# Optimization experiments

Measured on AMD Instinct MI355X. Metric: run time of the kernel, lower is better.

The kernel has to match this reference:

```python
import jax, jax.numpy as jnp
import numpy as np

L, B, T, D, H, F, V = 4, 2, 1024, 1024, 16, 4096, 32000
DH = D // H
POWER = 4
EPS = 1e-6


def _anorm(x, gain):
    # y = g * x / (mean(|x|) + eps)  (L1 'diamond' norm)
    return gain * (x / (jnp.mean(jnp.abs(x), axis=-1, keepdims=True) + EPS))


def _rational_softmax(x):
    s = x / (jnp.abs(x) + 1.0)          # squash to (-1, 1)
    p = ((s + 1.0) * 0.5) ** POWER      # shift to (0,1), sharpen
    return p / (jnp.sum(p, axis=-1, keepdims=True) + EPS)


def setup_inputs() -> dict:
    key = jax.random.key(0)
    ks = jax.random.split(key, 12)
    w = 0.02  # weight scale for stability
    return {
        "idx": jax.random.randint(ks[0], (B, T), 0, V),
        "tok_emb": jax.random.normal(ks[1], (V, D), jnp.float32) * w,
        "pos_emb": jax.random.normal(ks[2], (T, D), jnp.float32) * w,
        "Wq": jax.random.normal(ks[3], (L, D, D), jnp.float32) * w,
        "bq": jnp.zeros((L, D), jnp.float32),
        "Wk": jax.random.normal(ks[4], (L, D, D), jnp.float32) * w,
        "bk": jnp.zeros((L, D), jnp.float32),
        "Wv": jax.random.normal(ks[5], (L, D, D), jnp.float32) * w,
        "bv": jnp.zeros((L, D), jnp.float32),
        "Wo": jax.random.normal(ks[6], (L, D, D), jnp.float32) * w,
        "bo": jnp.zeros((L, D), jnp.float32),
        "score_gain": jnp.full((L,), 4.0, jnp.float32),
        "norm1_gain": jnp.ones((L, D), jnp.float32),
        "norm2_gain": jnp.ones((L, D), jnp.float32),
        "W1": jax.random.normal(ks[7], (L, D, F), jnp.float32) * w,
        "b1": jnp.zeros((L, F), jnp.float32),
        "W2": jax.random.normal(ks[8], (L, F, D), jnp.float32) * w,
        "b2": jnp.zeros((L, D), jnp.float32),
        "final_gain": jnp.ones((D,), jnp.float32),
        "Wlm": jax.random.normal(ks[9], (D, V), jnp.float32) * w,
        "blm": jnp.zeros((V,), jnp.float32),
    }


def _forward(idx, tok_emb, pos_emb, Wq, bq, Wk, bk, Wv, bv, Wo, bo,
             score_gain, norm1_gain, norm2_gain, W1, b1, W2, b2,
             final_gain, Wlm, blm):
    Bx, Tx = idx.shape
    x = tok_emb[idx] + pos_emb[:Tx]                 # [B,T,D]
    mask = jnp.triu(jnp.ones((Tx, Tx), bool), 1)    # causal mask (True = masked)
    for l in range(L):
        # --- algebraic attention ---
        h = _anorm(x, norm1_gain[l])
        q = (h @ Wq[l] + bq[l]).reshape(Bx, Tx, H, DH).transpose(0, 2, 1, 3)
        k = (h @ Wk[l] + bk[l]).reshape(Bx, Tx, H, DH).transpose(0, 2, 1, 3)
        v = (h @ Wv[l] + bv[l]).reshape(Bx, Tx, H, DH).transpose(0, 2, 1, 3)
        scores = jnp.einsum('bhqd,bhkd->bhqk', q, k)
        scores = scores - jnp.mean(scores, axis=-1, keepdims=True)
        mad = jnp.mean(jnp.abs(scores), axis=-1, keepdims=True) + EPS
        scores = (scores / mad) * score_gain[l]
        scores = jnp.where(mask, -1000.0, scores)
        attn = _rational_softmax(scores)
        o = jnp.einsum('bhqk,bhkd->bhqd', attn, v)
        o = o.transpose(0, 2, 1, 3).reshape(Bx, Tx, D)
        x = x + (o @ Wo[l] + bo[l])
        # --- FFN with algebraic ReLU ---
        h = _anorm(x, norm2_gain[l])
        h = jnp.maximum(h @ W1[l] + b1[l], 0.0)
        x = x + (h @ W2[l] + b2[l])
    x = _anorm(x, final_gain)
    return x @ Wlm + blm                            # [B,T,V] logits


def reference(idx, tok_emb, pos_emb, Wq, bq, Wk, bk, Wv, bv, Wo, bo,
              score_gain, norm1_gain, norm2_gain, W1, b1, W2, b2,
              final_gain, Wlm, blm):
    return _forward(idx, tok_emb, pos_emb, Wq, bq, Wk, bk, Wv, bv, Wo, bo,
                    score_gain, norm1_gain, norm2_gain, W1, b1, W2, b2,
                    final_gain, Wlm, blm)
```

## Files before the change

### kernel.cpp

```cpp
#include <hip/hip_runtime.h>

typedef unsigned short u16;
typedef __bf16 bf16x8 __attribute__((ext_vector_type(8)));
typedef float f32x4 __attribute__((ext_vector_type(4)));
typedef unsigned int u32;

#define EPSF 1e-6f

__device__ __forceinline__ u16 f2bf(float f) {
  union { float f; unsigned u; } un; un.f = f;
  unsigned r = un.u + 0x7FFFu + ((un.u >> 16) & 1u);
  return (u16)(r >> 16);
}

__device__ __forceinline__ float block_sum(float v) {
  #pragma unroll
  for (int off = 32; off > 0; off >>= 1) v += __shfl_xor(v, off, 64);
  __shared__ float ws[4];
  const int w = threadIdx.x >> 6;
  __syncthreads();
  if ((threadIdx.x & 63) == 0) ws[w] = v;
  __syncthreads();
  return ws[0] + ws[1] + ws[2] + ws[3];
}

__device__ __forceinline__ void lds_cp16(const void* g, void* l) {
  __builtin_amdgcn_global_load_lds(
      (__attribute__((address_space(1))) void*)g,
      (__attribute__((address_space(3))) void*)l, 16, 0, 0);
}

__global__ __launch_bounds__(256) void embed_norm(
    const int* __restrict__ idx, const float* __restrict__ tok,
    const float* __restrict__ pos, const float* __restrict__ gain,
    float* __restrict__ x, u16* __restrict__ h) {
  const int row = blockIdx.x;
  const int tpos = row & 1023;
  const int token = idx[row];
  const int d = threadIdx.x * 4;
  const float4 a = *(const float4*)(tok + (long)token * 1024 + d);
  const float4 b = *(const float4*)(pos + (long)tpos * 1024 + d);
  float4 o; o.x = a.x + b.x; o.y = a.y + b.y; o.z = a.z + b.z; o.w = a.w + b.w;
  *(float4*)(x + (long)row * 1024 + d) = o;
  float s = fabsf(o.x) + fabsf(o.y) + fabsf(o.z) + fabsf(o.w);
  s = block_sum(s);
  const float scale = 1.0f / (s * (1.0f / 1024.0f) + EPSF);
  const float4 g = *(const float4*)(gain + d);
  ushort4 ov;
  ov.x = f2bf(o.x * g.x * scale);
  ov.y = f2bf(o.y * g.y * scale);
  ov.z = f2bf(o.z * g.z * scale);
  ov.w = f2bf(o.w * g.w * scale);
  *(ushort4*)(h + (long)row * 1024 + d) = ov;
}

__global__ __launch_bounds__(512, 4) void attn_v5(
    const u16* __restrict__ qkv, const u16* __restrict__ v_t,
    u16* __restrict__ obuf, const float* __restrict__ score_gain, int l) {
  __shared__ float red1[2][4][16], red2[2][4][16], red3[2][4][16];
  __shared__ float Ured[2][4][16][68];
  __shared__ u16 Pl[8][640];
  const int qt = blockIdx.x, h = blockIdx.y, b = blockIdx.z;
  const int tid = threadIdx.x, w = tid >> 6, l64 = tid & 63;
  const int lq = l64 & 15, kgrp = l64 >> 4;
  const int wq = w >> 2, tq = w & 3;
  const int qglob = qt * 32 + wq * 16 + lq;
  const int qmax  = qt * 32 + wq * 16 + 15;
  const u16* Qg = qkv + (size_t)b * (1024 * 3072) + h * 64;
  const u16* Kg = Qg + 1024;
  const u16* Vt = v_t + (size_t)(b * 16 + h) * (64 * 1024);
  char* Pw = (char*)&Pl[w][0];

  bf16x8 qB0, qB1;
  {
    const u16* qp = Qg + (size_t)qglob * 3072 + (kgrp << 3);
    qB0 = *(const bf16x8*)qp;
    qB1 = *(const bf16x8*)(qp + 32);
  }

  f32x4 s[16];
  {
    const u16* Ktq = Kg + (size_t)(tq * 32 + lq) * 3072 + (kgrp << 3);
    #pragma unroll
    for (int tl = 0; tl < 16; tl++) {
      const int cst = ((tl >> 1) << 7) + ((tl & 1) << 4);
      const u16* kp = Ktq + (size_t)cst * 3072;
      const bf16x8 k0 = *(const bf16x8*)kp;
      const bf16x8 k1 = *(const bf16x8*)(kp + 32);
      f32x4 d = {0.f, 0.f, 0.f, 0.f};
      d = __builtin_amdgcn_mfma_f32_16x16x32_bf16(k0, qB0, d, 0, 0, 0);
      d = __builtin_amdgcn_mfma_f32_16x16x32_bf16(k1, qB1, d, 0, 0, 0);
      s[tl] = d;
    }
  }

  float ssum = 0.f;
  #pragma unroll
  for (int tl = 0; tl < 16; tl++)
    ssum += (s[tl][0] + s[tl][1]) + (s[tl][2] + s[tl][3]);
  ssum += __shfl_xor(ssum, 16, 64);
  ssum += __shfl_xor(ssum, 32, 64);
  if (l64 < 16) red1[wq][tq][l64] = ssum;
  __syncthreads();
  const float mean = (red1[wq][0][lq] + red1[wq][1][lq] +
                      red1[wq][2][lq] + red1[wq][3][lq]) * (1.0f / 1024.0f);

  float asum = 0.f;
  #pragma unroll
  for (int tl = 0; tl < 16; tl++)
    asum += fabsf(s[tl][0] - mean) + fabsf(s[tl][1] - mean) +
            fabsf(s[tl][2] - mean) + fabsf(s[tl][3] - mean);
  asum += __shfl_xor(asum, 16, 64);
  asum += __shfl_xor(asum, 32, 64);
  if (l64 < 16) red2[wq][tq][l64] = asum;
  __syncthreads();
  const float mad = (red2[wq][0][lq] + red2[wq][1][lq] +
                     red2[wq][2][lq] + red2[wq][3][lq]) * (1.0f / 1024.0f) + EPSF;
  const float gs = score_gain[l] / mad;

  float psum = 0.f;
  #pragma unroll
  for (int tl = 0; tl < 16; tl++) {
    const int tbase = tq * 32 + ((tl >> 1) << 7) + ((tl & 1) << 4);
    #pragma unroll
    for (int j = 0; j < 4; j++) {
      const int t = tbase + (kgrp << 2) + j;
      float sv = (s[tl][j] - mean) * gs;
      if (t > qglob) sv = -1000.0f;
      const float rr = sv / (fabsf(sv) + 1.0f);
      const float a1 = (rr + 1.0f) * 0.5f;
      const float a2 = a1 * a1;
      s[tl][j] = a2 * a2;
      psum += s[tl][j];
    }
  }

  f32x4 U[4] = {};
  {
    const u16* Vtq = Vt + (size_t)lq * 1024 + tq * 32 + (kgrp << 3);
    #pragma unroll
    for (int cc = 0; cc < 8; cc++) {
      const int t0 = tq * 32 + (cc << 7);
      if (t0 <= qmax) {
        bf16x8 vA[4];
        #pragma unroll
        for (int dt = 0; dt < 4; dt++)
          vA[dt] = *(const bf16x8*)(Vtq + (size_t)(dt << 4) * 1024 + (cc << 7));
        #pragma unroll
        for (int half = 0; half < 2; half++) {
          #pragma unroll
          for (int pr = 0; pr < 2; pr++) {
            const u32 pk = (u32)f2bf(s[2 * cc + half][pr * 2]) |
                           ((u32)f2bf(s[2 * cc + half][pr * 2 + 1]) << 16);
            *(u32*)(Pw + lq * 80 + half * 32 + (kgrp << 3) + (pr << 2)) = pk;
          }
        }
        asm volatile("s_waitcnt lgkmcnt(0)" ::: "memory");
        __builtin_amdgcn_sched_barrier(0);
        const bf16x8 pB = *(const bf16x8*)(Pw + lq * 80 + (kgrp << 4));
        #pragma unroll
        for (int dt = 0; dt < 4; dt++)
          U[dt] = __builtin_amdgcn_mfma_f32_16x16x32_bf16(vA[dt], pB, U[dt], 0, 0, 0);
      }
    }
  }

  psum += __shfl_xor(psum, 16, 64);
  psum += __shfl_xor(psum, 32, 64);
  if (l64 < 16) red3[wq][tq][l64] = psum;
  #pragma unroll
  for (int dt = 0; dt < 4; dt++)
    *(float4*)&Ured[wq][tq][lq][(dt << 4) + (kgrp << 2)] = *(const float4*)&U[dt];
  __syncthreads();

  {
    const int qq = tid >> 4, dhseg = (tid & 15) << 2;
    const int fwq = qq >> 4, flq = qq & 15;
    const float fps = red3[fwq][0][flq] + red3[fwq][1][flq] +
                      red3[fwq][2][flq] + red3[fwq][3][flq];
    const float oinv = 1.0f / (fps + EPSF);
    float4 u0 = *(const float4*)&Ured[fwq][0][flq][dhseg];
    const float4 u1 = *(const float4*)&Ured[fwq][1][flq][dhseg];
    const float4 u2 = *(const float4*)&Ured[fwq][2][flq][dhseg];
    const float4 u3 = *(const float4*)&Ured[fwq][3][flq][dhseg];
    u0.x = (u0.x + u1.x + u2.x + u3.x) * oinv;
    u0.y = (u0.y + u1.y + u2.y + u3.y) * oinv;
    u0.z = (u0.z + u1.z + u2.z + u3.z) * oinv;
    u0.w = (u0.w + u1.w + u2.w + u3.w) * oinv;
    ushort4 o;
    o.x = f2bf(u0.x); o.y = f2bf(u0.y); o.z = f2bf(u0.z); o.w = f2bf(u0.w);
    u16* dst = obuf + ((size_t)((b << 10) + qt * 32 + qq) << 10) + (h << 6) + dhseg;
    *(ushort4*)dst = o;
  }
}

__global__ void wconv_all(
    const float* __restrict__ Wq, const float* __restrict__ Wk,
    const float* __restrict__ Wv, const float* __restrict__ Wo,
    const float* __restrict__ W1, const float* __restrict__ W2,
    const float* __restrict__ Wlm,
    u16* __restrict__ wqkv_t, u16* __restrict__ wo_t,
    u16* __restrict__ w1_t, u16* __restrict__ w2_t, u16* __restrict__ wlm_t) {
  __shared__ float tile[64][65];
  const int bid = blockIdx.x;
  const float* src; u16* dst; int R, C, c0, r0;
  if (bid < 4096) {
    const int l = bid >> 10, m = (bid >> 8) & 3, t = bid & 255;
    if (m == 0)      src = Wq + (size_t)l * 1048576;
    else if (m == 1) src = Wk + (size_t)l * 1048576;
    else if (m == 2) src = Wv + (size_t)l * 1048576;
    else             src = Wo + (size_t)l * 1048576;
    dst = (m < 3) ? wqkv_t + ((size_t)l * 3072 + m * 1024) * 1024
                  : wo_t + (size_t)l * 1048576;
    R = 1024; C = 1024; c0 = (t & 15) << 6; r0 = (t >> 4) << 6;
  } else if (bid < 8192) {
    const int i = bid - 4096, l = i >> 10, t = i & 1023;
    src = W1 + (size_t)l * 4194304; dst = w1_t + (size_t)l * 4194304;
    R = 1024; C = 4096; c0 = (t & 63) << 6; r0 = (t >> 6) << 6;
  } else if (bid < 12288) {
    const int i = bid - 8192, l = i >> 10, t = i & 1023;
    src = W2 + (size_t)l * 4194304; dst = w2_t + (size_t)l * 4194304;
    R = 4096; C = 1024; c0 = (t & 15) << 6; r0 = (t >> 4) << 6;
  } else {
    const int i = bid - 12288;
    src = Wlm; dst = wlm_t;
    R = 1024; C = 32000; c0 = (i % 500) << 6; r0 = (i / 500) << 6;
  }
  const int tx = threadIdx.x, ty = threadIdx.y;
  const int cg = (tx & 15) << 2;
  const int rg = tx >> 4;
  #pragma unroll
  for (int i = 0; i < 4; i++) {
    const int row = i * 16 + ty * 4 + rg;
    const float4 v = *(const float4*)&src[(long)(r0 + row) * C + c0 + cg];
    tile[row][cg] = v.x; tile[row][cg + 1] = v.y;
    tile[row][cg + 2] = v.z; tile[row][cg + 3] = v.w;
  }
  __syncthreads();
  #pragma unroll
  for (int i = 0; i < 4; i++) {
    const int c = i * 16 + ty * 4 + rg;
    ushort4 o;
    o.x = f2bf(tile[cg][c]);     o.y = f2bf(tile[cg + 1][c]);
    o.z = f2bf(tile[cg + 2][c]); o.w = f2bf(tile[cg + 3][c]);
    *(ushort4*)&dst[(long)(c0 + c) * R + r0 + cg] = o;
  }
}

__global__ __launch_bounds__(256) void bias_concat(
    const float* __restrict__ bq, const float* __restrict__ bk,
    const float* __restrict__ bv, float* __restrict__ out) {
  const int i = blockIdx.x * 256 + threadIdx.x;
  const int l = i / 3072, j = i % 3072;
  float v;
  if (j < 1024)      v = bq[l * 1024 + j];
  else if (j < 2048) v = bk[l * 1024 + j - 1024];
  else               v = bv[l * 1024 + j - 2048];
  out[i] = v;
}

template <int NPART>
__global__ __launch_bounds__(256) void reduce_norm(
    const float* __restrict__ part, const float* __restrict__ bias,
    float* __restrict__ x, const float* __restrict__ gain,
    u16* __restrict__ h) {
  const int row = blockIdx.x, c = threadIdx.x * 4;
  float4 acc = *(const float4*)(part + (size_t)row * 1024 + c);
  #pragma unroll
  for (int i = 1; i < NPART; i++) {
    const float4 pi = *(const float4*)(part + (size_t)(row + i * 2048) * 1024 + c);
    acc.x += pi.x; acc.y += pi.y; acc.z += pi.z; acc.w += pi.w;
  }
  const float4 bb = *(const float4*)(bias + c);
  float4 xv = *(float4*)(x + (size_t)row * 1024 + c);
  xv.x += acc.x + bb.x;
  xv.y += acc.y + bb.y;
  xv.z += acc.z + bb.z;
  xv.w += acc.w + bb.w;
  *(float4*)(x + (size_t)row * 1024 + c) = xv;
  float s = fabsf(xv.x) + fabsf(xv.y) + fabsf(xv.z) + fabsf(xv.w);
  s = block_sum(s);
  const float scale = 1.0f / (s * (1.0f / 1024.0f) + EPSF);
  const float4 g = *(const float4*)(gain + c);
  ushort4 o;
  o.x = f2bf(xv.x * g.x * scale);
  o.y = f2bf(xv.y * g.y * scale);
  o.z = f2bf(xv.z * g.z * scale);
  o.w = f2bf(xv.w * g.w * scale);
  *(ushort4*)(h + (size_t)row * 1024 + c) = o;
}

template <bool OUT_BF16, bool BIAS>
__global__ __launch_bounds__(512) void gemm256_8p(
    const u16* __restrict__ A, long lda,
    const u16* __restrict__ Bt, long ldb,
    void* __restrict__ Cv, long ldc,
    const float* __restrict__ bias,
    int M, int N, int K, int nTM) {
  __shared__ u16 lds[65536];
  const int nwg = gridDim.x;
  const int qx = nwg >> 3, rx = nwg & 7;
  const int xcd = blockIdx.x & 7, seq = blockIdx.x >> 3;
  const int wg = (xcd < rx ? xcd * (qx + 1) : rx * (qx + 1) + (xcd - rx) * qx) + seq;
  const int tm = wg % nTM, tn = wg / nTM;
  const int rowA0 = tm * 256, rowB0 = tn * 256;

  const int t = threadIdx.x, w = t >> 6, l = t & 63;
  const int lrow = l & 15, kgrp = l >> 4;
  const int wr = w >> 2, wc = w & 3;

  const int srow = (w << 3) + (l >> 3);
  const int scol = (((l & 7) ^ (l >> 3)) << 3);
  const u16* Ab = A + (long)rowA0 * lda;
  const u16* Bb = Bt + (long)rowB0 * ldb;
  char* ldsB = (char*)lds;
  const int wb = w << 10;

  auto stg = [&](int db, int region, int q, int k0) {
    const u16* srcb = region ? Bb : Ab;
    const long ld = region ? ldb : lda;
    lds_cp16(srcb + (long)(q * 64 + srow) * ld + k0 + scol,
             ldsB + db * 65536 + region * 32768 + q * 8192 + wb);
  };

  const int aswz = lrow & 7;
  const int kc0 = (kgrp ^ aswz) << 4;
  const int kc1 = ((4 + kgrp) ^ aswz) << 4;
  int arow[8], brow[4];
  #pragma unroll
  for (int m = 0; m < 8; m++) arow[m] = (wr * 128 + m * 16 + lrow) * 128;
  #pragma unroll
  for (int n = 0; n < 4; n++) brow[n] = 32768 + (wc * 64 + n * 16 + lrow) * 128;

  f32x4 acc[8][4] = {};
  const int NKT = K >> 6;
  const int NIT = NKT >> 1;

  #pragma unroll
  for (int q = 0; q < 4; q++) stg(0, 0, q, 0);
  #pragma unroll
  for (int q = 0; q < 4; q++) stg(0, 1, q, 0);
  #pragma unroll
  for (int q = 0; q < 4; q++) stg(1, 0, q, 64);
  #pragma unroll
  for (int q = 0; q < 4; q++) stg(1, 1, q, 64);

  for (int it = 0; it < NIT; ++it) {
    const int kt = it << 1;
    const bool sok = (it < NIT - 1);
    const int k2 = (kt + 2) << 6, k3 = (kt + 3) << 6;
    bf16x8 a0[4], ah0[4], b0[4], a1[4], ah1[4], b1[4];

    #pragma unroll
    for (int half = 0; half < 2; half++) {
      const int dbB = half * 65536;
      const int kn = half ? k3 : k2;

      if (half == 0 || sok) asm volatile("s_waitcnt vmcnt(8)" ::: "memory");
      else                  asm volatile("s_waitcnt vmcnt(0)" ::: "memory");
      __builtin_amdgcn_sched_barrier(0);
      __builtin_amdgcn_s_barrier();

      #pragma unroll
      for (int m = 0; m < 4; m++) a0[m]  = *(const bf16x8*)(ldsB + dbB + arow[m] + kc0);
      #pragma unroll
      for (int n = 0; n < 4; n++) b0[n]  = *(const bf16x8*)(ldsB + dbB + brow[n] + kc0);
      #pragma unroll
      for (int m = 0; m < 4; m++) ah0[m] = *(const bf16x8*)(ldsB + dbB + arow[m + 4] + kc0);
      asm volatile("s_waitcnt lgkmcnt(4)" ::: "memory");
      __builtin_amdgcn_sched_barrier(0);
      __builtin_amdgcn_s_setprio(1);
      #pragma unroll
      for (int m = 0; m < 4; m++)
        #pragma unroll
        for (int n = 0; n < 4; n++)
          acc[m][n] = __builtin_amdgcn_mfma_f32_16x16x32_bf16(a0[m], b0[n], acc[m][n], 0, 0, 0);
      __builtin_amdgcn_s_setprio(0);
      __builtin_amdgcn_sched_barrier(0);

      #pragma unroll
      for (int m = 0; m < 4; m++) a1[m]  = *(const bf16x8*)(ldsB + dbB + arow[m] + kc1);
      #pragma unroll
      for (int n = 0; n < 4; n++) b1[n]  = *(const bf16x8*)(ldsB + dbB + brow[n] + kc1);
      #pragma unroll
      for (int m = 0; m < 4; m++) ah1[m] = *(const bf16x8*)(ldsB + dbB + arow[m + 4] + kc1);
      asm volatile("s_waitcnt lgkmcnt(12)" ::: "memory");
      __builtin_amdgcn_sched_barrier(0);
      __builtin_amdgcn_s_setprio(1);
      #pragma unroll
      for (int m = 0; m < 4; m++)
        #pragma unroll
        for (int n = 0; n < 4; n++)
          acc[m + 4][n] = __builtin_amdgcn_mfma_f32_16x16x32_bf16(ah0[m], b0[n], acc[m + 4][n], 0, 0, 0);
      __builtin_amdgcn_s_setprio(0);
      asm volatile("s_waitcnt lgkmcnt(0)" ::: "memory");
      __builtin_amdgcn_sched_barrier(0);
      __builtin_amdgcn_s_barrier();

      if (sok) {
        #pragma unroll
        for (int q = 0; q < 4; q++) stg(half, 0, q, kn);
      }
      __builtin_amdgcn_sched_barrier(0);
      __builtin_amdgcn_s_setprio(1);
      #pragma unroll
      for (int m = 0; m < 4; m++)
        #pragma unroll
        for (int n = 0; n < 4; n++)
          acc[m][n] = __builtin_amdgcn_mfma_f32_16x16x32_bf16(a1[m], b1[n], acc[m][n], 0, 0, 0);
      __builtin_amdgcn_s_setprio(0);
      __builtin_amdgcn_sched_barrier(0);

      if (sok) {
        #pragma unroll
        for (int q = 0; q < 4; q++) stg(half, 1, q, kn);
      }
      __builtin_amdgcn_sched_barrier(0);
      __builtin_amdgcn_s_setprio(1);
      #pragma unroll
      for (int m = 0; m < 4; m++)
        #pragma unroll
        for (int n = 0; n < 4; n++)
          acc[m + 4][n] = __builtin_amdgcn_mfma_f32_16x16x32_bf16(ah1[m], b1[n], acc[m + 4][n], 0, 0, 0);
      __builtin_amdgcn_s_setprio(0);
      __builtin_amdgcn_sched_barrier(0);
    }
  }

  float bvv[4];
  #pragma unroll
  for (int n = 0; n < 4; n++)
    bvv[n] = BIAS ? bias[rowB0 + wc * 64 + n * 16 + lrow] : 0.0f;
  #pragma unroll
  for (int m = 0; m < 8; m++) {
    const int row = rowA0 + wr * 128 + m * 16 + kgrp * 4;
    #pragma unroll
    for (int n = 0; n < 4; n++) {
      const int col = rowB0 + wc * 64 + n * 16 + lrow;
      #pragma unroll
      for (int j = 0; j < 4; j++) {
        float v = acc[m][n][j] + bvv[n];
        const long off = (long)(row + j) * ldc + col;
        if (OUT_BF16) ((u16*)Cv)[off] = f2bf(v);
        else          ((float*)Cv)[off] = v;
      }
    }
  }
}

template <bool OUT_BF16, bool BIAS, bool RELU, bool RESID, bool VTOUT>
__global__ __launch_bounds__(256) void gemm128p(
    const u16* __restrict__ A, long lda, long sA,
    const u16* __restrict__ Bt, long ldb, long sB,
    void* __restrict__ Cv, long ldc, long sC,
    const float* __restrict__ bias, const float* __restrict__ resid,
    u16* __restrict__ vtout,
    int M, int N, int K, int nTM) {
  __shared__ u16 lds[32768];
  const int nwg = gridDim.x;
  const int qx = nwg >> 3, rx = nwg & 7;
  const int xcd = blockIdx.x & 7, seq = blockIdx.x >> 3;
  const int wg = (xcd < rx ? xcd * (qx + 1) : rx * (qx + 1) + (xcd - rx) * qx) + seq;
  const int tm = wg % nTM, tn = wg / nTM;
  const int batch = blockIdx.y;
  A  += (long)batch * sA;
  Bt += (long)batch * sB;
  const int rowA0 = tm * 128, rowB0 = tn * 128;
  const int t = threadIdx.x, w = t >> 6, l = t & 63;
  const int lrow = l & 15, kgrp = l >> 4;
  const int wr = (w >> 1) << 6, wc = (w & 1) << 6;

  const int srow = t >> 2;
  const int scol = ((t & 3) ^ ((t >> 3) & 3)) * 8;
  const u16* Asrc = A + (long)(rowA0 + srow) * lda + scol;
  const u16* Bsrc = Bt + (long)(rowB0 + srow) * ldb + scol;
  char* ldsB = (char*)lds;
  const int wbase = w * 1024;

  const int swz8 = (kgrp ^ ((lrow >> 1) & 3)) * 8;
  const int aoff = (wr + lrow) * 32 + swz8;
  const int boff = 4096 + (wc + lrow) * 32 + swz8;

  f32x4 acc[4][4] = {};
  const int NT = K >> 5;

  #pragma unroll
  for (int pt = 0; pt < 3; pt++) {
    const int k0 = pt << 5;
    const int bb = pt * 16384;
    lds_cp16(Asrc + k0,                   ldsB + bb + wbase);
    lds_cp16(Asrc + (long)64 * lda + k0,  ldsB + bb + 4096 + wbase);
    lds_cp16(Bsrc + k0,                   ldsB + bb + 8192 + wbase);
    lds_cp16(Bsrc + (long)64 * ldb + k0,  ldsB + bb + 12288 + wbase);
  }

  for (int tt = 0; tt < NT; tt++) {
    const int rem = NT - 1 - tt;
    if (rem >= 2)      asm volatile("s_waitcnt vmcnt(8)" ::: "memory");
    else if (rem == 1) asm volatile("s_waitcnt vmcnt(4)" ::: "memory");
    else               asm volatile("s_waitcnt vmcnt(0)" ::: "memory");
    __builtin_amdgcn_sched_barrier(0);
    __builtin_amdgcn_s_barrier();

    const u16* buf = lds + (tt & 3) * 8192;
    const int stage = tt + 3 < NT;
    const int k0n = (tt + 3) << 5;
    const int bbn = ((tt + 3) & 3) * 16384;

    bf16x8 aF[4], bF[4];
    #pragma unroll
    for (int m = 0; m < 4; m++) aF[m] = *(const bf16x8*)(buf + aoff + m * 512);
    #pragma unroll
    for (int n = 0; n < 4; n++) bF[n] = *(const bf16x8*)(buf + boff + n * 512);
    if (stage) {
      lds_cp16(Asrc + k0n,                  ldsB + bbn + wbase);
      lds_cp16(Asrc + (long)64 * lda + k0n, ldsB + bbn + 4096 + wbase);
      lds_cp16(Bsrc + k0n,                  ldsB + bbn + 8192 + wbase);
      lds_cp16(Bsrc + (long)64 * ldb + k0n, ldsB + bbn + 12288 + wbase);
    }
    asm volatile("s_waitcnt lgkmcnt(0)" ::: "memory");
    __builtin_amdgcn_sched_barrier(0);
    __builtin_amdgcn_s_setprio(1);
    #pragma unroll
    for (int m = 0; m < 4; m++)
      #pragma unroll
      for (int n = 0; n < 4; n++)
        acc[m][n] = __builtin_amdgcn_mfma_f32_16x16x32_bf16(aF[m], bF[n], acc[m][n], 0, 0, 0);
    __builtin_amdgcn_s_setprio(0);
  }

  if (VTOUT && rowB0 >= 2048) {
    __syncthreads();
    #pragma unroll
    for (int m = 0; m < 4; m++) {
      #pragma unroll
      for (int n = 0; n < 4; n++) {
        const int c = wc + n * 16 + lrow;
        const int r = wr + m * 16 + (kgrp << 2);
        ushort4 pk;
        float v0 = acc[m][n][0], v1 = acc[m][n][1], v2 = acc[m][n][2], v3 = acc[m][n][3];
        if (BIAS) {
          const float bv = bias[rowB0 + c];
          v0 += bv; v1 += bv; v2 += bv; v3 += bv;
        }
        pk.x = f2bf(v0); pk.y = f2bf(v1); pk.z = f2bf(v2); pk.w = f2bf(v3);
        *(ushort4*)&lds[c * 136 + r] = pk;
      }
    }
    __syncthreads();
    {
      const int c = t >> 1, half = t & 1;
      const int dh = c & 63;
      const int h = ((rowB0 - 2048) >> 6) + (c >> 6);
      const int bb2 = rowA0 >> 10, t0 = rowA0 & 1023;
      u16* dst = vtout + (((size_t)(bb2 * 16 + h)) << 16) + ((size_t)dh << 10) +
                 t0 + half * 64;
      #pragma unroll
      for (int k = 0; k < 8; k++)
        *(bf16x8*)(dst + k * 8) = *(const bf16x8*)&lds[c * 136 + half * 64 + k * 8];
    }
  } else {
    const long coff = (long)batch * sC;
    #pragma unroll
    for (int m = 0; m < 4; m++) {
      #pragma unroll
      for (int n = 0; n < 4; n++) {
        const int col = rowB0 + wc + n * 16 + lrow;
        #pragma unroll
        for (int j = 0; j < 4; j++) {
          const int row = rowA0 + wr + m * 16 + (kgrp << 2) + j;
          float v = acc[m][n][j];
          if (BIAS) v += bias[col];
          if (RELU) v = fmaxf(v, 0.0f);
          const long off = coff + (long)row * ldc + col;
          if (RESID) v += resid[off];
          if (OUT_BF16) ((u16*)Cv)[off] = f2bf(v);
          else          ((float*)Cv)[off] = v;
        }
      }
    }
  }
}

extern "C" void kernel_launch(void* const* d_in, const int* in_sizes, int n_in,
                              void* d_out, int out_size, void* d_ws, size_t ws_size,
                              hipStream_t stream) {
  constexpr int Lc = 4, Tc = 1024, Dc = 1024, Hc = 16, Fc = 4096, DHc = 64;
  const int M = 2 * Tc;

  const int*   idxp       = (const int*)  d_in[0];
  const float* tok_emb    = (const float*)d_in[1];
  const float* pos_emb    = (const float*)d_in[2];
  const float* Wq         = (const float*)d_in[3];
  const float* bq         = (const float*)d_in[4];
  const float* Wk         = (const float*)d_in[5];
  const float* bk         = (const float*)d_in[6];
  const float* Wv         = (const float*)d_in[7];
  const float* bv         = (const float*)d_in[8];
  const float* Wo         = (const float*)d_in[9];
  const float* bo         = (const float*)d_in[10];
  const float* score_gain = (const float*)d_in[11];
  const float* norm1_gain = (const float*)d_in[12];
  const float* norm2_gain = (const float*)d_in[13];
  const float* W1         = (const float*)d_in[14];
  const float* b1         = (const float*)d_in[15];
  const float* W2         = (const float*)d_in[16];
  const float* b2         = (const float*)d_in[17];
  const float* final_gain = (const float*)d_in[18];
  const float* Wlm        = (const float*)d_in[19];
  const float* blm        = (const float*)d_in[20];

  char* p = (char*)d_ws;
  auto alloc = [&](size_t n) { char* r = p; p += (n + 255) & ~(size_t)255; return r; };
  u16*  wqkv_t = (u16*) alloc((size_t)Lc * 3072 * 1024 * 2);
  u16*  wo_t   = (u16*) alloc((size_t)Lc * 1024 * 1024 * 2);
  u16*  w1_t   = (u16*) alloc((size_t)Lc * 4096 * 1024 * 2);
  u16*  w2_t   = (u16*) alloc((size_t)Lc * 1024 * 4096 * 2);
  u16*  wlm_t  = (u16*) alloc((size_t)32000 * 1024 * 2);
  float* bqkv  = (float*)alloc((size_t)Lc * 3072 * 4);
  float* x     = (float*)alloc((size_t)M * 1024 * 4);
  u16*  hbuf   = (u16*) alloc((size_t)M * 1024 * 2);
  u16*  qkv    = (u16*) alloc((size_t)M * 3072 * 2);
  u16*  v_t    = (u16*) alloc((size_t)2 * Hc * DHc * Tc * 2);
  u16*  obuf   = (u16*) alloc((size_t)M * 1024 * 2);
  u16*  ffh    = (u16*) alloc((size_t)M * 4096 * 2);
  float* fpart = (float*)alloc((size_t)4 * M * 1024 * 4);

  wconv_all<<<20288, dim3(64, 4), 0, stream>>>(Wq, Wk, Wv, Wo, W1, W2, Wlm,
                                               wqkv_t, wo_t, w1_t, w2_t, wlm_t);
  bias_concat<<<48, 256, 0, stream>>>(bq, bk, bv, bqkv);
  embed_norm<<<M, 256, 0, stream>>>(idxp, tok_emb, pos_emb, norm1_gain, x, hbuf);

  for (int l = 0; l < Lc; l++) {
    gemm128p<true, true, false, false, true><<<dim3(16 * 24, 1), 256, 0, stream>>>(
        hbuf, 1024, 0, wqkv_t + (size_t)l * 3072 * 1024, 1024, 0,
        qkv, 3072, 0, bqkv + (size_t)l * 3072, nullptr, v_t, M, 3072, 1024, 16);

    attn_v5<<<dim3(32, 16, 2), 512, 0, stream>>>(qkv, v_t, obuf, score_gain, l);

    gemm128p<false, false, false, false, false><<<dim3(128, 2), 256, 0, stream>>>(
        obuf, 1024, 512, wo_t + (size_t)l * 1024 * 1024, 1024, 512,
        fpart, 1024, (long)M * 1024, nullptr, nullptr, nullptr, M, 1024, 512, 16);
    reduce_norm<2><<<M, 256, 0, stream>>>(fpart, bo + (size_t)l * Dc, x,
                                          norm2_gain + (size_t)l * Dc, hbuf);
    gemm128p<true, true, true, false, false><<<dim3(16 * 32, 1), 256, 0, stream>>>(
        hbuf, 1024, 0, w1_t + (size_t)l * Fc * Dc, 1024, 0,
        ffh, 4096, 0, b1 + (size_t)l * Fc, nullptr, nullptr, M, 4096, 1024, 16);
    gemm128p<false, false, false, false, false><<<dim3(128, 4), 256, 0, stream>>>(
        ffh, 4096, 1024, w2_t + (size_t)l * Dc * Fc, 4096, 1024,
        fpart, 1024, (long)M * 1024, nullptr, nullptr, nullptr, M, 1024, 1024, 16);
    const float* gnext = (l < Lc - 1) ? (norm1_gain + (size_t)(l + 1) * Dc) : final_gain;
    reduce_norm<4><<<M, 256, 0, stream>>>(fpart, b2 + (size_t)l * Dc, x, gnext, hbuf);
  }

  gemm256_8p<false, true><<<dim3(1000), 512, 0, stream>>>(
      hbuf, 1024, wlm_t, 1024,
      d_out, 32000, blm, M, 32000, 1024, 8);
}
```

Before: 1.150 ms.

## Restructure LM-head GEMM pipeline into finer-grained staged quarter-tile loads

```diff
diff --git a/kernel.cpp b/kernel.cpp
--- a/kernel.cpp
+++ b/kernel.cpp
@@ -291,7 +291,7 @@
 }
 
 template <bool OUT_BF16, bool BIAS>
-__global__ __launch_bounds__(512) void gemm256_8p(
+__global__ __launch_bounds__(512, 1) void gemm256_m201(
     const u16* __restrict__ A, long lda,
     const u16* __restrict__ Bt, long ldb,
     void* __restrict__ Cv, long ldc,
@@ -309,122 +309,113 @@
   const int lrow = l & 15, kgrp = l >> 4;
   const int wr = w >> 2, wc = w & 3;
 
-  const int srow = (w << 3) + (l >> 3);
-  const int scol = (((l & 7) ^ (l >> 3)) << 3);
   const u16* Ab = A + (long)rowA0 * lda;
   const u16* Bb = Bt + (long)rowB0 * ldb;
   char* ldsB = (char*)lds;
+
+  const int scol = (((l & 3) ^ ((l >> 3) & 3)) << 3);
+  const int srow0 = (w << 4) + (l >> 2);
   const int wb = w << 10;
-
-  auto stg = [&](int db, int region, int q, int k0) {
-    const u16* srcb = region ? Bb : Ab;
-    const long ld = region ? ldb : lda;
-    lds_cp16(srcb + (long)(q * 64 + srow) * ld + k0 + scol,
-             ldsB + db * 65536 + region * 32768 + q * 8192 + wb);
+  auto stg = [&](int h) {
+    const int tile = h >> 2, q = h & 3;
+    const int db = tile & 1, khalf = q >> 1, isB = q & 1;
+    const u16* srcb = isB ? Bb : Ab;
+    const long ld = isB ? ldb : lda;
+    const int k0 = (tile << 6) + (khalf << 5);
+    char* dst = ldsB + db * 65536 + q * 16384 + wb;
+    lds_cp16(srcb + (long)srow0 * ld + k0 + scol,         dst);
+    lds_cp16(srcb + (long)(srow0 + 128) * ld + k0 + scol, dst + 8192);
   };
 
-  const int aswz = lrow & 7;
-  const int kc0 = (kgrp ^ aswz) << 4;
-  const int kc1 = ((4 + kgrp) ^ aswz) << 4;
-  int arow[8], brow[4];
-  #pragma unroll
-  for (int m = 0; m < 8; m++) arow[m] = (wr * 128 + m * 16 + lrow) * 128;
-  #pragma unroll
-  for (int n = 0; n < 4; n++) brow[n] = 32768 + (wc * 64 + n * 16 + lrow) * 128;
+  const int swz = (kgrp ^ ((lrow >> 1) & 3)) << 4;
+  int Aoff[8], Boff[4];
+  #pragma unroll
+  for (int m = 0; m < 8; m++) Aoff[m] = ((wr * 128 + m * 16 + lrow) << 6) + swz;
+  #pragma unroll
+  for (int n = 0; n < 4; n++) Boff[n] = ((wc * 64 + n * 16 + lrow) << 6) + swz;
 
   f32x4 acc[8][4] = {};
-  const int NKT = K >> 6;
-  const int NIT = NKT >> 1;
-
-  #pragma unroll
-  for (int q = 0; q < 4; q++) stg(0, 0, q, 0);
-  #pragma unroll
-  for (int q = 0; q < 4; q++) stg(0, 1, q, 0);
-  #pragma unroll
-  for (int q = 0; q < 4; q++) stg(1, 0, q, 64);
-  #pragma unroll
-  for (int q = 0; q < 4; q++) stg(1, 1, q, 64);
-
-  for (int it = 0; it < NIT; ++it) {
-    const int kt = it << 1;
-    const bool sok = (it < NIT - 1);
-    const int k2 = (kt + 2) << 6, k3 = (kt + 3) << 6;
-    bf16x8 a0[4], ah0[4], b0[4], a1[4], ah1[4], b1[4];
-
-    #pragma unroll
-    for (int half = 0; half < 2; half++) {
-      const int dbB = half * 65536;
-      const int kn = half ? k3 : k2;
-
-      if (half == 0 || sok) asm volatile("s_waitcnt vmcnt(8)" ::: "memory");
-      else                  asm volatile("s_waitcnt vmcnt(0)" ::: "memory");
-      __builtin_amdgcn_sched_barrier(0);
-      __builtin_amdgcn_s_barrier();
-
-      #pragma unroll
-      for (int m = 0; m < 4; m++) a0[m]  = *(const bf16x8*)(ldsB + dbB + arow[m] + kc0);
-      #pragma unroll
-      for (int n = 0; n < 4; n++) b0[n]  = *(const bf16x8*)(ldsB + dbB + brow[n] + kc0);
-      #pragma unroll
-      for (int m = 0; m < 4; m++) ah0[m] = *(const bf16x8*)(ldsB + dbB + arow[m + 4] + kc0);
-      asm volatile("s_waitcnt lgkmcnt(4)" ::: "memory");
-      __builtin_amdgcn_sched_barrier(0);
-      __builtin_amdgcn_s_setprio(1);
-      #pragma unroll
-      for (int m = 0; m < 4; m++)
-        #pragma unroll
-        for (int n = 0; n < 4; n++)
-          acc[m][n] = __builtin_amdgcn_mfma_f32_16x16x32_bf16(a0[m], b0[n], acc[m][n], 0, 0, 0);
-      __builtin_amdgcn_s_setprio(0);
-      __builtin_amdgcn_sched_barrier(0);
-
-      #pragma unroll
-      for (int m = 0; m < 4; m++) a1[m]  = *(const bf16x8*)(ldsB + dbB + arow[m] + kc1);
-      #pragma unroll
-      for (int n = 0; n < 4; n++) b1[n]  = *(const bf16x8*)(ldsB + dbB + brow[n] + kc1);
-      #pragma unroll
-      for (int m = 0; m < 4; m++) ah1[m] = *(const bf16x8*)(ldsB + dbB + arow[m + 4] + kc1);
-      asm volatile("s_waitcnt lgkmcnt(12)" ::: "memory");
-      __builtin_amdgcn_sched_barrier(0);
-      __builtin_amdgcn_s_setprio(1);
-      #pragma unroll
-      for (int m = 0; m < 4; m++)
-        #pragma unroll
-        for (int n = 0; n < 4; n++)
-          acc[m + 4][n] = __builtin_amdgcn_mfma_f32_16x16x32_bf16(ah0[m], b0[n], acc[m + 4][n], 0, 0, 0);
-      __builtin_amdgcn_s_setprio(0);
-      asm volatile("s_waitcnt lgkmcnt(0)" ::: "memory");
-      __builtin_amdgcn_sched_barrier(0);
-      __builtin_amdgcn_s_barrier();
-
-      if (sok) {
-        #pragma unroll
-        for (int q = 0; q < 4; q++) stg(half, 0, q, kn);
-      }
-      __builtin_amdgcn_sched_barrier(0);
-      __builtin_amdgcn_s_setprio(1);
-      #pragma unroll
-      for (int m = 0; m < 4; m++)
-        #pragma unroll
-        for (int n = 0; n < 4; n++)
-          acc[m][n] = __builtin_amdgcn_mfma_f32_16x16x32_bf16(a1[m], b1[n], acc[m][n], 0, 0, 0);
-      __builtin_amdgcn_s_setprio(0);
-      __builtin_amdgcn_sched_barrier(0);
-
-      if (sok) {
-        #pragma unroll
-        for (int q = 0; q < 4; q++) stg(half, 1, q, kn);
-      }
-      __builtin_amdgcn_sched_barrier(0);
-      __builtin_amdgcn_s_setprio(1);
-      #pragma unroll
-      for (int m = 0; m < 4; m++)
-        #pragma unroll
-        for (int n = 0; n < 4; n++)
-          acc[m + 4][n] = __builtin_amdgcn_mfma_f32_16x16x32_bf16(ah1[m], b1[n], acc[m + 4][n], 0, 0, 0);
-      __builtin_amdgcn_s_setprio(0);
-      __builtin_amdgcn_sched_barrier(0);
-    }
+  const int NT = K >> 6;
+  const int NH = NT << 2;
+
+  #pragma unroll
+  for (int h = 0; h < 6; h++) stg(h);
+
+  for (int k = 0; k < NT; k++) {
+    char* base = ldsB + (k & 1) * 65536;
+    const int g0 = k << 2;
+    bf16x8 aF[4], bF[4];
+
+    if (k == NT - 1) asm volatile("s_waitcnt vmcnt(0)" ::: "memory");
+    else             asm volatile("s_waitcnt vmcnt(4)" ::: "memory");
+    __builtin_amdgcn_sched_barrier(0);
+    __builtin_amdgcn_s_barrier();
+    #pragma unroll
+    for (int m = 0; m < 4; m++) aF[m] = *(const bf16x8*)(base + Aoff[m]);
+    #pragma unroll
+    for (int n = 0; n < 4; n++) bF[n] = *(const bf16x8*)(base + 16384 + Boff[n]);
+    if (g0 + 6 < NH) stg(g0 + 6);
+    asm volatile("s_waitcnt lgkmcnt(0)" ::: "memory");
+    __builtin_amdgcn_sched_barrier(0);
+    __builtin_amdgcn_s_setprio(1);
+    #pragma unroll
+    for (int m = 0; m < 4; m++)
+      #pragma unroll
+      for (int n = 0; n < 4; n++)
+        acc[m][n] = __builtin_amdgcn_mfma_f32_16x16x32_bf16(aF[m], bF[n], acc[m][n], 0, 0, 0);
+    __builtin_amdgcn_s_setprio(0);
+    __builtin_amdgcn_sched_barrier(0);
+    __builtin_amdgcn_s_barrier();
+
+    #pragma unroll
+    for (int m = 0; m < 4; m++) aF[m] = *(const bf16x8*)(base + Aoff[m + 4]);
+    if (g0 + 7 < NH) stg(g0 + 7);
+    asm volatile("s_waitcnt lgkmcnt(0)" ::: "memory");
+    __builtin_amdgcn_sched_barrier(0);
+    __builtin_amdgcn_s_setprio(1);
+    #pragma unroll
+    for (int m = 0; m < 4; m++)
+      #pragma unroll
+      for (int n = 0; n < 4; n++)
+        acc[m + 4][n] = __builtin_amdgcn_mfma_f32_16x16x32_bf16(aF[m], bF[n], acc[m + 4][n], 0, 0, 0);
+    __builtin_amdgcn_s_setprio(0);
+    __builtin_amdgcn_sched_barrier(0);
+    __builtin_amdgcn_s_barrier();
+
+    asm volatile("s_waitcnt vmcnt(8)" ::: "memory");
+    __builtin_amdgcn_sched_barrier(0);
+    __builtin_amdgcn_s_barrier();
+    #pragma unroll
+    for (int m = 0; m < 4; m++) aF[m] = *(const bf16x8*)(base + 32768 + Aoff[m]);
+    #pragma unroll
+    for (int n = 0; n < 4; n++) bF[n] = *(const bf16x8*)(base + 49152 + Boff[n]);
+    if (g0 + 8 < NH) stg(g0 + 8);
+    asm volatile("s_waitcnt lgkmcnt(0)" ::: "memory");
+    __builtin_amdgcn_sched_barrier(0);
+    __builtin_amdgcn_s_setprio(1);
+    #pragma unroll
+    for (int m = 0; m < 4; m++)
+      #pragma unroll
+      for (int n = 0; n < 4; n++)
+        acc[m][n] = __builtin_amdgcn_mfma_f32_16x16x32_bf16(aF[m], bF[n], acc[m][n], 0, 0, 0);
+    __builtin_amdgcn_s_setprio(0);
+    __builtin_amdgcn_sched_barrier(0);
+    __builtin_amdgcn_s_barrier();
+
+    #pragma unroll
+    for (int m = 0; m < 4; m++) aF[m] = *(const bf16x8*)(base + 32768 + Aoff[m + 4]);
+    if (g0 + 9 < NH) stg(g0 + 9);
+    asm volatile("s_waitcnt lgkmcnt(0)" ::: "memory");
+    __builtin_amdgcn_sched_barrier(0);
+    __builtin_amdgcn_s_setprio(1);
+    #pragma unroll
+    for (int m = 0; m < 4; m++)
+      #pragma unroll
+      for (int n = 0; n < 4; n++)
+        acc[m + 4][n] = __builtin_amdgcn_mfma_f32_16x16x32_bf16(aF[m], bF[n], acc[m + 4][n], 0, 0, 0);
+    __builtin_amdgcn_s_setprio(0);
+    __builtin_amdgcn_sched_barrier(0);
+    __builtin_amdgcn_s_barrier();
   }
 
   float bvv[4];
@@ -653,7 +644,7 @@
     reduce_norm<4><<<M, 256, 0, stream>>>(fpart, b2 + (size_t)l * Dc, x, gnext, hbuf);
   }
 
-  gemm256_8p<false, true><<<dim3(1000), 512, 0, stream>>>(
+  gemm256_m201<false, true><<<dim3(1000), 512, 0, stream>>>(
       hbuf, 1024, wlm_t, 1024,
       d_out, 32000, blm, M, 32000, 1024, 8);
 }
```

After: 980.3 us. -14.7%, faster.
